# Optimization experiments

Hardware: AMD Instinct MI355X
Metric: run time of the kernel (lower is better)

Reference implementation:

```python
import jax, jax.numpy as jnp
import numpy as np

N_VARS = 1_000_000
NB, NS, NL = 400_000, 300_000, 200_000  # binary / small-int / large-int counts
C_CLS = 16
N_CON = 500_000
E = 16_000_000
LP_SOL_COL = 8
BIAS_COL = 1
LAMBDA_MEAN, LAMBDA_MAX = 1.0, 0.1


def setup_inputs() -> dict:
    key = jax.random.key(0)
    ks = jax.random.split(key, 10)
    # disjoint variable index partitions: [0,NB) bin, [NB,NB+NS) small int,
    # [NB+NS,NB+NS+NL) large int, rest continuous (var_types==0)
    idx_bin = jnp.arange(NB, dtype=jnp.int64)
    idx_int_small = jnp.arange(NB, NB + NS, dtype=jnp.int64)
    idx_int_large = jnp.arange(NB + NS, NB + NS + NL, dtype=jnp.int64)
    var_types = jnp.concatenate([
        jnp.ones(NB, dtype=jnp.int64),                 # binary
        jnp.full((NS + NL,), 2, dtype=jnp.int64),      # integer
        jnp.zeros(N_VARS - NB - NS - NL, dtype=jnp.int64),  # continuous
    ])
    edge_indices = jnp.stack([
        jax.random.randint(ks[0], (E,), 0, N_CON, dtype=jnp.int64),
        jax.random.randint(ks[1], (E,), 0, N_VARS, dtype=jnp.int64),
    ])
    return {
        'prob_bin': jax.random.uniform(ks[2], (NB, 1), jnp.float32),
        'logits_int_small': jax.random.normal(ks[3], (NS, C_CLS), jnp.float32),
        'int_small_offsets': jax.random.normal(ks[4], (NS,), jnp.float32),
        'pred_int_large': jax.random.normal(ks[5], (NL, 1), jnp.float32),
        'edge_features': jax.random.normal(ks[6], (E, 1), jnp.float32),
        'constraint_features': jax.random.normal(ks[7], (N_CON, 8), jnp.float32),
        'variable_features': jax.random.normal(ks[8], (N_VARS, 16), jnp.float32),
        'idx_bin': idx_bin,
        'idx_int_small': idx_int_small,
        'idx_int_large': idx_int_large,
        'var_types': var_types,
        'edge_indices': edge_indices,
        'n_vars': N_VARS,
    }


def _build_x(prob_bin, logits_int_small, int_small_offsets, pred_int_large,
             variable_features, idx_bin, idx_int_small, idx_int_large,
             var_types, n_vars):
    x = jnp.zeros((n_vars,), dtype=prob_bin.dtype)
    x = x.at[idx_bin].set(prob_bin[:, 0])
    # expected value of small-int class distribution
    probs = jax.nn.softmax(logits_int_small, axis=-1)                  # [NS, C]
    class_values = jnp.arange(logits_int_small.shape[1], dtype=probs.dtype)
    expected = probs @ class_values + int_small_offsets                # [NS]
    x = x.at[idx_int_small].set(expected)
    x = x.at[idx_int_large].set(pred_int_large[:, 0])
    # continuous vars take detached LP solution values
    lp_vals = jax.lax.stop_gradient(variable_features[:, LP_SOL_COL])
    x = jnp.where(var_types == 0, lp_vals, x)
    return x


def reference(prob_bin, logits_int_small, int_small_offsets, pred_int_large,
              edge_features, constraint_features, variable_features,
              idx_bin, idx_int_small, idx_int_large, var_types,
              edge_indices, n_vars):
    x = _build_x(prob_bin, logits_int_small, int_small_offsets, pred_int_large,
                 variable_features, idx_bin, idx_int_small, idx_int_large,
                 var_types, n_vars)
    n_cons = constraint_features.shape[0]
    # sparse A @ x: gather variable values along edges, scale, scatter-add per constraint
    weighted = edge_features.reshape(-1) * x[edge_indices[1]]          # [E]
    Ax = jax.ops.segment_sum(weighted, edge_indices[0], num_segments=n_cons)
    violation = jax.nn.relu(Ax - constraint_features[:, BIAS_COL])     # [N_con]
    mean_viol = violation.mean()
    max_viol = violation.max()
    n_violated = jnp.sum(violation > 1e-6)
    penalty = LAMBDA_MEAN * mean_viol + LAMBDA_MAX * max_viol
    return penalty, mean_viol, max_viol, n_violated
```

## Files before the change

### kernel.cpp

```cpp
#include <hip/hip_runtime.h>


#define BSHIFT 14
#define BROWS  (1 << BSHIFT)
#define NBUCK_MAX 32
#define CHUNK 8192
#define ROUNDS (CHUNK / 1024)
#define BUF 128
#define THRESH 48
#define SPLIT 16

typedef int   iv4 __attribute__((ext_vector_type(4)));
typedef float fv4 __attribute__((ext_vector_type(4)));

__device__ inline unsigned pack_rec(int loc, float v) {
    unsigned f = __float_as_uint(v);
    unsigned b = (f + 0x7FFFu + ((f >> 16) & 1u)) >> 16;
    return ((unsigned)loc << 16) | b;
}


__global__ __launch_bounds__(256) void k_build_hist(
    const float* __restrict__ prob_bin, const int* __restrict__ idx_bin, int NB, int gBin,
    const float* __restrict__ logits, const float* __restrict__ offs,
    const int* __restrict__ idx_small, int NS, int gSml,
    const float* __restrict__ pred, const int* __restrict__ idx_large, int NL, int gLrg,
    const int* __restrict__ vt, const float* __restrict__ vf, int NV, int gCnt,
    const int* __restrict__ rows, int* __restrict__ counts,
    int nchunks, int E, int nbuck,
    float* __restrict__ x, float* __restrict__ acc)
{
    int blk = blockIdx.x, tid = threadIdx.x;
    if (blk == 0 && tid < 4) reinterpret_cast<unsigned*>(acc)[tid] = 0u;

    if (blk < gBin) {
        int i = blk * 256 + tid;
        if (i < NB) x[idx_bin[i]] = prob_bin[i];
        return;
    }
    blk -= gBin;
    if (blk < gSml) {
        int i = blk * 256 + tid;
        if (i < NS) {
            const fv4* lp = reinterpret_cast<const fv4*>(logits + (size_t)i * 16);
            fv4 v0 = lp[0], v1 = lp[1], v2 = lp[2], v3 = lp[3];
            float l[16] = {v0.x, v0.y, v0.z, v0.w, v1.x, v1.y, v1.z, v1.w,
                           v2.x, v2.y, v2.z, v2.w, v3.x, v3.y, v3.z, v3.w};
            float m = l[0];
#pragma unroll
            for (int j = 1; j < 16; ++j) m = fmaxf(m, l[j]);
            float s = 0.f, ws = 0.f;
#pragma unroll
            for (int j = 0; j < 16; ++j) {
                float e = expf(l[j] - m);
                s += e;
                ws += e * (float)j;
            }
            x[idx_small[i]] = ws / s + offs[i];
        }
        return;
    }
    blk -= gSml;
    if (blk < gLrg) {
        int i = blk * 256 + tid;
        if (i < NL) x[idx_large[i]] = pred[i];
        return;
    }
    blk -= gLrg;
    if (blk < gCnt) {
        int v = blk * 256 + tid;
        if (v < NV && vt[v] == 0) x[v] = vf[(size_t)v * 16 + 8];
        return;
    }
    blk -= gCnt;
    __shared__ int h[NBUCK_MAX];
    if (tid < NBUCK_MAX) h[tid] = 0;
    __syncthreads();
    int e4max = E >> 2;
    int base4 = blk * (CHUNK / 4);
#pragma unroll
    for (int k = 0; k < ROUNDS; ++k) {
        int i4 = base4 + k * 256 + tid;
        if (i4 < e4max) {
            iv4 r = reinterpret_cast<const iv4*>(rows)[i4];
            atomicAdd(&h[r.x >> BSHIFT], 1);
            atomicAdd(&h[r.y >> BSHIFT], 1);
            atomicAdd(&h[r.z >> BSHIFT], 1);
            atomicAdd(&h[r.w >> BSHIFT], 1);
        }
    }
    if (blk == 0 && tid < (E & 3))
        atomicAdd(&h[rows[(E & ~3) + tid] >> BSHIFT], 1);
    __syncthreads();
    if (tid < nbuck) counts[(size_t)tid * nchunks + blk] = h[tid];
}


__global__ void k_scanchunks(const int* __restrict__ counts, int* __restrict__ off,
                             int* __restrict__ total, int nchunks) {
    int b = blockIdx.x, lane = threadIdx.x;
    int carry = 0;
    for (int i0 = 0; i0 < nchunks; i0 += 64) {
        int i = i0 + lane;
        int v = (i < nchunks) ? counts[(size_t)b * nchunks + i] : 0;
        int orig = v;
#pragma unroll
        for (int o = 1; o < 64; o <<= 1) {
            int t = __shfl_up(v, o, 64);
            if (lane >= o) v += t;
        }
        if (i < nchunks) off[(size_t)b * nchunks + i] = carry + v - orig;
        carry += __shfl(v, 63, 64);
    }
    if (lane == 0) total[b] = carry;
}

__global__ void k_bases(const int* __restrict__ total, int* __restrict__ base, int nbuck) {
    if (blockIdx.x == 0 && threadIdx.x == 0) {
        int s = 0;
        for (int b = 0; b < nbuck; ++b) { base[b] = s; s += total[b]; }
        base[nbuck] = s;
    }
}


__global__ __launch_bounds__(256) void k_scatter3(const int* __restrict__ rows,
                                                  const int* __restrict__ cols,
                                                  const float* __restrict__ ef,
                                                  const float* __restrict__ x,
                                                  const int* __restrict__ off,
                                                  const int* __restrict__ base,
                                                  unsigned* __restrict__ recs,
                                                  int nchunks, int E, int nbuck) {
    __shared__ unsigned bufr[NBUCK_MAX][BUF];
    __shared__ int fill[NBUCK_MAX];
    __shared__ int done[NBUCK_MAX];
    __shared__ int cbase[NBUCK_MAX];

    int tid = threadIdx.x, chunk = blockIdx.x;
    if (tid < NBUCK_MAX) {
        fill[tid] = 0;
        done[tid] = 0;
        cbase[tid] = (tid < nbuck) ? base[tid] + off[(size_t)tid * nchunks + chunk] : 0;
    }
    __syncthreads();

    int e4max = E >> 2;
    int base4 = chunk * (CHUNK / 4);
    int wid = tid >> 6, lane = tid & 63;

    iv4 r, c; fv4 f;
    bool valid;
    {
        int i4 = base4 + tid;
        valid = i4 < e4max;
        if (valid) {
            r = __builtin_nontemporal_load(reinterpret_cast<const iv4*>(rows) + i4);
            c = __builtin_nontemporal_load(reinterpret_cast<const iv4*>(cols) + i4);
            f = __builtin_nontemporal_load(reinterpret_cast<const fv4*>(ef) + i4);
        }
    }

    for (int k = 0; k < ROUNDS; ++k) {
        iv4 rr = r, cc = c; fv4 ff = f;
        bool val = valid;
        if (k + 1 < ROUNDS) {
            int i4 = base4 + (k + 1) * 256 + tid;
            valid = i4 < e4max;
            if (valid) {
                r = __builtin_nontemporal_load(reinterpret_cast<const iv4*>(rows) + i4);
                c = __builtin_nontemporal_load(reinterpret_cast<const iv4*>(cols) + i4);
                f = __builtin_nontemporal_load(reinterpret_cast<const fv4*>(ef) + i4);
            }
        }
        if (val) {
            int   ra[4] = {rr.x, rr.y, rr.z, rr.w};
            int   ca[4] = {cc.x, cc.y, cc.z, cc.w};
            float fa[4] = {ff.x, ff.y, ff.z, ff.w};
#pragma unroll
            for (int j = 0; j < 4; ++j) {
                int b = ra[j] >> BSHIFT;
                unsigned rec = pack_rec(ra[j] & (BROWS - 1), fa[j] * x[ca[j]]);
                int pos = atomicAdd(&fill[b], 1);
                if (pos < BUF) bufr[b][pos] = rec;
                else recs[cbase[b] + done[b] + pos] = rec;
            }
        }
        if (k == ROUNDS - 1 && chunk == 0 && tid < (E & 3)) {
            int e = (E & ~3) + tid;
            int rrow = rows[e];
            int b = rrow >> BSHIFT;
            unsigned rec = pack_rec(rrow & (BROWS - 1), ef[e] * x[cols[e]]);
            int pos = atomicAdd(&fill[b], 1);
            if (pos < BUF) bufr[b][pos] = rec;
            else recs[cbase[b] + done[b] + pos] = rec;
        }
        __syncthreads();
        bool last = (k == ROUNDS - 1);
        for (int b = wid; b < nbuck; b += 4) {
            int fl = fill[b];
            if (fl == 0) continue;
            if (fl >= THRESH || last) {
                int n = fl < BUF ? fl : BUF;
                int g = cbase[b] + done[b];
                for (int j = lane; j < n; j += 64) recs[g + j] = bufr[b][j];
                if (lane == 0) { done[b] += fl; fill[b] = 0; }
            }
        }
        __syncthreads();
    }
}


__global__ __launch_bounds__(256) void k_accum(const unsigned* __restrict__ recs,
                                               const int* __restrict__ base,
                                               float* __restrict__ partial) {
    __shared__ float tile[BROWS];
    int tid = threadIdx.x;
    int b = blockIdx.x / SPLIT, s = blockIdx.x % SPLIT;
    for (int i = tid; i < BROWS; i += 256) tile[i] = 0.f;
    __syncthreads();
    int lo = base[b], hi = base[b + 1];
    int len = hi - lo, per = (len + SPLIT - 1) / SPLIT;
    int s0 = lo + s * per;
    int s1 = s0 + per; if (s1 > hi) s1 = hi;
    int i = s0 + tid;
    for (; i + 768 < s1; i += 1024) {
        unsigned r0 = __builtin_nontemporal_load(recs + i);
        unsigned r1 = __builtin_nontemporal_load(recs + i + 256);
        unsigned r2 = __builtin_nontemporal_load(recs + i + 512);
        unsigned r3 = __builtin_nontemporal_load(recs + i + 768);
        atomicAdd(&tile[r0 >> 16], __uint_as_float((r0 & 0xFFFFu) << 16));
        atomicAdd(&tile[r1 >> 16], __uint_as_float((r1 & 0xFFFFu) << 16));
        atomicAdd(&tile[r2 >> 16], __uint_as_float((r2 & 0xFFFFu) << 16));
        atomicAdd(&tile[r3 >> 16], __uint_as_float((r3 & 0xFFFFu) << 16));
    }
    for (; i < s1; i += 256) {
        unsigned rr = recs[i];
        atomicAdd(&tile[rr >> 16], __uint_as_float((rr & 0xFFFFu) << 16));
    }
    __syncthreads();
    float* out = partial + ((size_t)blockIdx.x << BSHIFT);
    for (int j = tid; j < BROWS; j += 256) out[j] = tile[j];
}


__global__ __launch_bounds__(256) void k_reduce_fin(const float* __restrict__ partial,
                                                    const float* __restrict__ cf,
                                                    float* __restrict__ acc,
                                                    float* __restrict__ out,
                                                    int ncon, int nblocks) {
    float lsum = 0.f, lmax = 0.f;
    unsigned lcnt = 0;
    int stride = gridDim.x * blockDim.x;
    for (int c = blockIdx.x * blockDim.x + threadIdx.x; c < ncon; c += stride) {
        int b = c >> BSHIFT, i = c & (BROWS - 1);
        const float* p = partial + (((size_t)b * SPLIT) << BSHIFT) + i;
        float v = 0.f;
#pragma unroll
        for (int s = 0; s < SPLIT; ++s)
            v += __builtin_nontemporal_load(p + ((size_t)s << BSHIFT));
        v -= cf[(size_t)c * 8 + 1];
        v = v > 0.f ? v : 0.f;
        lsum += v;
        lmax = fmaxf(lmax, v);
        lcnt += (v > 1e-6f) ? 1u : 0u;
    }
#pragma unroll
    for (int o = 32; o > 0; o >>= 1) {
        lsum += __shfl_down(lsum, o);
        lmax = fmaxf(lmax, __shfl_down(lmax, o));
        lcnt += __shfl_down(lcnt, o);
    }
    __shared__ float ssum[4];
    __shared__ float smax[4];
    __shared__ unsigned scnt[4];
    int lane = threadIdx.x & 63, wid = threadIdx.x >> 6;
    if (lane == 0) { ssum[wid] = lsum; smax[wid] = lmax; scnt[wid] = lcnt; }
    __syncthreads();
    if (threadIdx.x == 0) {
        float bs = 0.f, bm = 0.f;
        unsigned bc = 0;
        int nw = (blockDim.x + 63) >> 6;
        for (int w = 0; w < nw; ++w) { bs += ssum[w]; bm = fmaxf(bm, smax[w]); bc += scnt[w]; }
        atomicAdd(&acc[0], bs);
        atomicMax(reinterpret_cast<unsigned*>(acc) + 1, __float_as_uint(bm));
        atomicAdd(reinterpret_cast<unsigned*>(acc) + 2, bc);
        __threadfence();
        unsigned t = atomicAdd(reinterpret_cast<unsigned*>(acc) + 3, 1u);
        if (t == (unsigned)(nblocks - 1)) {
            float sum   = atomicAdd(&acc[0], 0.f);
            unsigned mb = atomicMax(reinterpret_cast<unsigned*>(acc) + 1, 0u);
            unsigned ct = atomicAdd(reinterpret_cast<unsigned*>(acc) + 2, 0u);
            float mean = sum / (float)ncon;
            float mx = __uint_as_float(mb);
            out[0] = mean + 0.1f * mx;
            out[1] = mean;
            out[2] = mx;
            out[3] = (float)ct;
        }
    }
}


__global__ void k_scatter_f(const float* __restrict__ src, const int* __restrict__ idx,
                            float* __restrict__ x, int n) {
    int i = blockIdx.x * blockDim.x + threadIdx.x;
    if (i < n) x[idx[i]] = src[i];
}

__global__ void k_edges(const float* __restrict__ ef, const int* __restrict__ rows,
                        const int* __restrict__ cols, const float* __restrict__ x,
                        float* __restrict__ Ax, int e4, int E) {
    int stride = gridDim.x * blockDim.x;
    int gid = blockIdx.x * blockDim.x + threadIdx.x;
    for (int i = gid; i < e4; i += stride) {
        fv4 f = reinterpret_cast<const fv4*>(ef)[i];
        iv4 r = reinterpret_cast<const iv4*>(rows)[i];
        iv4 c = reinterpret_cast<const iv4*>(cols)[i];
        atomicAdd(&Ax[r.x], f.x * x[c.x]);
        atomicAdd(&Ax[r.y], f.y * x[c.y]);
        atomicAdd(&Ax[r.z], f.z * x[c.z]);
        atomicAdd(&Ax[r.w], f.w * x[c.w]);
    }
    for (int e = e4 * 4 + gid; e < E; e += stride)
        atomicAdd(&Ax[rows[e]], ef[e] * x[cols[e]]);
}

__global__ void k_reduce_ax(const float* __restrict__ Ax, const float* __restrict__ cf,
                            float* __restrict__ acc, int ncon) {
    float lsum = 0.f, lmax = 0.f;
    unsigned lcnt = 0;
    int stride = gridDim.x * blockDim.x;
    for (int c = blockIdx.x * blockDim.x + threadIdx.x; c < ncon; c += stride) {
        float v = Ax[c] - cf[(size_t)c * 8 + 1];
        v = v > 0.f ? v : 0.f;
        lsum += v;
        lmax = fmaxf(lmax, v);
        lcnt += (v > 1e-6f) ? 1u : 0u;
    }
#pragma unroll
    for (int o = 32; o > 0; o >>= 1) {
        lsum += __shfl_down(lsum, o);
        lmax = fmaxf(lmax, __shfl_down(lmax, o));
        lcnt += __shfl_down(lcnt, o);
    }
    __shared__ float ssum[4];
    __shared__ float smax[4];
    __shared__ unsigned scnt[4];
    int lane = threadIdx.x & 63, wid = threadIdx.x >> 6;
    if (lane == 0) { ssum[wid] = lsum; smax[wid] = lmax; scnt[wid] = lcnt; }
    __syncthreads();
    if (threadIdx.x == 0) {
        float bs = 0.f, bm = 0.f;
        unsigned bc = 0;
        int nw = (blockDim.x + 63) >> 6;
        for (int w = 0; w < nw; ++w) { bs += ssum[w]; bm = fmaxf(bm, smax[w]); bc += scnt[w]; }
        atomicAdd(&acc[0], bs);
        atomicMax(reinterpret_cast<unsigned*>(acc) + 1, __float_as_uint(bm));
        atomicAdd(reinterpret_cast<unsigned*>(acc) + 2, bc);
    }
}

__global__ void k_final(const float* __restrict__ acc, float* __restrict__ out, int ncon) {
    if (blockIdx.x == 0 && threadIdx.x == 0) {
        float sum = acc[0];
        float mx = __uint_as_float(reinterpret_cast<const unsigned*>(acc)[1]);
        unsigned cnt = reinterpret_cast<const unsigned*>(acc)[2];
        float mean = sum / (float)ncon;
        out[0] = mean + 0.1f * mx;
        out[1] = mean;
        out[2] = mx;
        out[3] = (float)cnt;
    }
}

__global__ void k_small_int_f(const float* __restrict__ logits, const float* __restrict__ offs,
                              const int* __restrict__ idx, float* __restrict__ x, int n) {
    int i = blockIdx.x * blockDim.x + threadIdx.x;
    if (i >= n) return;
    const fv4* lp = reinterpret_cast<const fv4*>(logits + (size_t)i * 16);
    fv4 v0 = lp[0], v1 = lp[1], v2 = lp[2], v3 = lp[3];
    float l[16] = {v0.x, v0.y, v0.z, v0.w, v1.x, v1.y, v1.z, v1.w,
                   v2.x, v2.y, v2.z, v2.w, v3.x, v3.y, v3.z, v3.w};
    float m = l[0];
#pragma unroll
    for (int j = 1; j < 16; ++j) m = fmaxf(m, l[j]);
    float s = 0.f, ws = 0.f;
#pragma unroll
    for (int j = 0; j < 16; ++j) {
        float e = expf(l[j] - m);
        s += e;
        ws += e * (float)j;
    }
    x[idx[i]] = ws / s + offs[i];
}

__global__ void k_continuous_f(const int* __restrict__ vt, const float* __restrict__ vf,
                               float* __restrict__ x, int n) {
    int v = blockIdx.x * blockDim.x + threadIdx.x;
    if (v < n && vt[v] == 0) x[v] = vf[(size_t)v * 16 + 8];
}


extern "C" void kernel_launch(void* const* d_in, const int* in_sizes, int n_in,
                              void* d_out, int out_size, void* d_ws, size_t ws_size,
                              hipStream_t stream) {
    const float* prob_bin     = (const float*)d_in[0];
    const float* logits_small = (const float*)d_in[1];
    const float* offs_small   = (const float*)d_in[2];
    const float* pred_large   = (const float*)d_in[3];
    const float* edge_feat    = (const float*)d_in[4];
    const float* cons_feat    = (const float*)d_in[5];
    const float* var_feat     = (const float*)d_in[6];
    const int*   idx_bin      = (const int*)d_in[7];
    const int*   idx_small    = (const int*)d_in[8];
    const int*   idx_large    = (const int*)d_in[9];
    const int*   var_types    = (const int*)d_in[10];
    const int*   edge_indices = (const int*)d_in[11];

    const int NB    = in_sizes[0];
    const int NS    = in_sizes[2];
    const int NL    = in_sizes[3];
    const int E     = in_sizes[4];
    const int NCON  = in_sizes[5] / 8;
    const int NVARS = in_sizes[10];

    const int* rows = edge_indices;
    const int* cols = edge_indices + E;

    const int nbuck   = (NCON + BROWS - 1) >> BSHIFT;
    const int nchunks = (E + CHUNK - 1) / CHUNK;

    char* w = (char*)d_ws;
    size_t o = 0;
    auto take = [&](size_t bytes) -> char* {
        char* p = w + o;
        o = (o + bytes + 255) & ~(size_t)255;
        return p;
    };
    float*    x       = (float*)take((size_t)NVARS * 4);
    unsigned* recs    = (unsigned*)take((size_t)E * 4);
    float*    partial = (float*)take((size_t)nbuck * SPLIT * BROWS * 4);
    int*      counts  = (int*)take((size_t)nbuck * nchunks * 4);
    int*      off     = (int*)take((size_t)nbuck * nchunks * 4);
    int*      base    = (int*)take((size_t)(nbuck + 1) * 4);
    int*      total   = (int*)take((size_t)nbuck * 4);
    float*    acc     = (float*)take(16);

    bool sorted_path = (o <= ws_size) && (nbuck <= NBUCK_MAX);

    const int B = 256;

    if (sorted_path) {
        const int gBin = (NB + B - 1) / B;
        const int gSml = (NS + B - 1) / B;
        const int gLrg = (NL + B - 1) / B;
        const int gCnt = (NVARS + B - 1) / B;
        const int grid1 = gBin + gSml + gLrg + gCnt + nchunks;

        k_build_hist<<<grid1, B, 0, stream>>>(
            prob_bin, idx_bin, NB, gBin,
            logits_small, offs_small, idx_small, NS, gSml,
            pred_large, idx_large, NL, gLrg,
            var_types, var_feat, NVARS, gCnt,
            rows, counts, nchunks, E, nbuck, x, acc);
        k_scanchunks<<<nbuck, 64, 0, stream>>>(counts, off, total, nchunks);
        k_bases<<<1, 64, 0, stream>>>(total, base, nbuck);
        k_scatter3<<<nchunks, B, 0, stream>>>(rows, cols, edge_feat, x, off, base,
                                              recs, nchunks, E, nbuck);
        k_accum<<<nbuck * SPLIT, B, 0, stream>>>(recs, base, partial);
        const int rblocks = 1024;
        k_reduce_fin<<<rblocks, B, 0, stream>>>(partial, cons_feat, acc, (float*)d_out,
                                                NCON, rblocks);
    } else {
        float* accf = (float*)((char*)d_ws + (size_t)NVARS * 4);
        float* Ax   = accf + 4;
        (void)hipMemsetAsync(accf, 0, (size_t)(4 + NCON) * sizeof(float), stream);
        k_scatter_f<<<(NB + B - 1) / B, B, 0, stream>>>(prob_bin, idx_bin, x, NB);
        k_small_int_f<<<(NS + B - 1) / B, B, 0, stream>>>(logits_small, offs_small, idx_small, x, NS);
        k_scatter_f<<<(NL + B - 1) / B, B, 0, stream>>>(pred_large, idx_large, x, NL);
        k_continuous_f<<<(NVARS + B - 1) / B, B, 0, stream>>>(var_types, var_feat, x, NVARS);
        k_edges<<<2048, B, 0, stream>>>(edge_feat, rows, cols, x, Ax, E / 4, E);
        k_reduce_ax<<<1024, B, 0, stream>>>(Ax, cons_feat, accf, NCON);
        k_final<<<1, 64, 0, stream>>>(accf, (float*)d_out, NCON);
    }
}
```

Measured before the change: 313.3 us.

## Compute bf16 edge products in histogram pass and scan with wide blocks

The x-building work is split out of the histogram kernel. The histogram pass now also gathers x, multiplies by the edge weights and writes packed bf16 products, so the scatter pass reads 8 bytes per 4 edges instead of re-reading cols and edge features and gathering x. The chunk scan uses 1024-thread blocks and folds in the bucket-base computation, and bucket segments are padded to multiples of 4 so the accumulate kernel can use vector loads. This adds a product buffer write and read and a second edge pass that loads cols, features and x, in exchange for a lighter scatter pass and fewer launches.

```diff
diff --git a/kernel.cpp b/kernel.cpp
--- a/kernel.cpp
+++ b/kernel.cpp
@@ -10,24 +10,23 @@
 #define THRESH 48
 #define SPLIT 16
 
-typedef int   iv4 __attribute__((ext_vector_type(4)));
-typedef float fv4 __attribute__((ext_vector_type(4)));
-
-__device__ inline unsigned pack_rec(int loc, float v) {
+typedef int      iv4 __attribute__((ext_vector_type(4)));
+typedef float    fv4 __attribute__((ext_vector_type(4)));
+typedef unsigned uv2 __attribute__((ext_vector_type(2)));
+typedef unsigned uv4 __attribute__((ext_vector_type(4)));
+
+__device__ inline unsigned bf16bits(float v) {
     unsigned f = __float_as_uint(v);
-    unsigned b = (f + 0x7FFFu + ((f >> 16) & 1u)) >> 16;
-    return ((unsigned)loc << 16) | b;
-}
-
-
-__global__ __launch_bounds__(256) void k_build_hist(
+    return (f + 0x7FFFu + ((f >> 16) & 1u)) >> 16;
+}
+
+
+__global__ __launch_bounds__(256) void k_build_x(
     const float* __restrict__ prob_bin, const int* __restrict__ idx_bin, int NB, int gBin,
     const float* __restrict__ logits, const float* __restrict__ offs,
     const int* __restrict__ idx_small, int NS, int gSml,
     const float* __restrict__ pred, const int* __restrict__ idx_large, int NL, int gLrg,
-    const int* __restrict__ vt, const float* __restrict__ vf, int NV, int gCnt,
-    const int* __restrict__ rows, int* __restrict__ counts,
-    int nchunks, int E, int nbuck,
+    const int* __restrict__ vt, const float* __restrict__ vf, int NV,
     float* __restrict__ x, float* __restrict__ acc)
 {
     int blk = blockIdx.x, tid = threadIdx.x;
@@ -67,69 +66,106 @@
         return;
     }
     blk -= gLrg;
-    if (blk < gCnt) {
+    {
         int v = blk * 256 + tid;
         if (v < NV && vt[v] == 0) x[v] = vf[(size_t)v * 16 + 8];
-        return;
-    }
-    blk -= gCnt;
-    __shared__ int h[NBUCK_MAX];
-    if (tid < NBUCK_MAX) h[tid] = 0;
+    }
+}
+
+
+template <bool PROD>
+__global__ __launch_bounds__(256) void k_hist_prod(const int* __restrict__ rows,
+                                                   const int* __restrict__ cols,
+                                                   const float* __restrict__ ef,
+                                                   const float* __restrict__ x,
+                                                   int* __restrict__ counts,
+                                                   unsigned* __restrict__ prods,
+                                                   int nchunks, int E, int nbuck) {
+    __shared__ int h[4][NBUCK_MAX];
+    int tid = threadIdx.x, chunk = blockIdx.x, wid = tid >> 6, lane = tid & 63;
+    if (lane < NBUCK_MAX) h[wid][lane] = 0;
     __syncthreads();
     int e4max = E >> 2;
-    int base4 = blk * (CHUNK / 4);
+    int b4 = chunk * (CHUNK / 4);
 #pragma unroll
     for (int k = 0; k < ROUNDS; ++k) {
-        int i4 = base4 + k * 256 + tid;
+        int i4 = b4 + k * 256 + tid;
         if (i4 < e4max) {
-            iv4 r = reinterpret_cast<const iv4*>(rows)[i4];
-            atomicAdd(&h[r.x >> BSHIFT], 1);
-            atomicAdd(&h[r.y >> BSHIFT], 1);
-            atomicAdd(&h[r.z >> BSHIFT], 1);
-            atomicAdd(&h[r.w >> BSHIFT], 1);
-        }
-    }
-    if (blk == 0 && tid < (E & 3))
-        atomicAdd(&h[rows[(E & ~3) + tid] >> BSHIFT], 1);
-    __syncthreads();
-    if (tid < nbuck) counts[(size_t)tid * nchunks + blk] = h[tid];
-}
-
-
-__global__ void k_scanchunks(const int* __restrict__ counts, int* __restrict__ off,
-                             int* __restrict__ total, int nchunks) {
-    int b = blockIdx.x, lane = threadIdx.x;
+            iv4 r = __builtin_nontemporal_load(reinterpret_cast<const iv4*>(rows) + i4);
+            atomicAdd(&h[wid][r.x >> BSHIFT], 1);
+            atomicAdd(&h[wid][r.y >> BSHIFT], 1);
+            atomicAdd(&h[wid][r.z >> BSHIFT], 1);
+            atomicAdd(&h[wid][r.w >> BSHIFT], 1);
+            if (PROD) {
+                iv4 c = __builtin_nontemporal_load(reinterpret_cast<const iv4*>(cols) + i4);
+                fv4 f = __builtin_nontemporal_load(reinterpret_cast<const fv4*>(ef) + i4);
+                unsigned p01 = bf16bits(f.x * x[c.x]) | (bf16bits(f.y * x[c.y]) << 16);
+                unsigned p23 = bf16bits(f.z * x[c.z]) | (bf16bits(f.w * x[c.w]) << 16);
+                uv2 p = {p01, p23};
+                __builtin_nontemporal_store(p, reinterpret_cast<uv2*>(prods) + i4);
+            }
+        }
+    }
+    if (chunk == 0 && tid < (E & 3)) {
+        int e = (E & ~3) + tid;
+        atomicAdd(&h[wid][rows[e] >> BSHIFT], 1);
+        if (PROD)
+            reinterpret_cast<unsigned short*>(prods)[e] =
+                (unsigned short)bf16bits(ef[e] * x[cols[e]]);
+    }
+    __syncthreads();
+    if (tid < nbuck)
+        counts[(size_t)tid * nchunks + chunk] = h[0][tid] + h[1][tid] + h[2][tid] + h[3][tid];
+}
+
+
+__global__ __launch_bounds__(1024) void k_scan(const int* __restrict__ counts,
+                                               int* __restrict__ off,
+                                               int* __restrict__ total, int nchunks) {
+    int b = blockIdx.x;
+    __shared__ int wtot[16];
+    __shared__ int wbase[16];
+    int tid = threadIdx.x, w = tid >> 6, lane = tid & 63;
+    int seg = (nchunks + 15) >> 4;
+    int lo = w * seg;
+    int hi = lo + seg; if (hi > nchunks) hi = nchunks;
+    const int* cb = counts + (size_t)b * nchunks;
+    int* ob = off + (size_t)b * nchunks;
     int carry = 0;
-    for (int i0 = 0; i0 < nchunks; i0 += 64) {
+    for (int i0 = lo; i0 < hi; i0 += 64) {
         int i = i0 + lane;
-        int v = (i < nchunks) ? counts[(size_t)b * nchunks + i] : 0;
+        int v = (i < hi) ? cb[i] : 0;
         int orig = v;
 #pragma unroll
         for (int o = 1; o < 64; o <<= 1) {
             int t = __shfl_up(v, o, 64);
             if (lane >= o) v += t;
         }
-        if (i < nchunks) off[(size_t)b * nchunks + i] = carry + v - orig;
+        if (i < hi) ob[i] = carry + v - orig;
         carry += __shfl(v, 63, 64);
     }
-    if (lane == 0) total[b] = carry;
-}
-
-__global__ void k_bases(const int* __restrict__ total, int* __restrict__ base, int nbuck) {
-    if (blockIdx.x == 0 && threadIdx.x == 0) {
+    if (lane == 0) wtot[w] = carry;
+    __syncthreads();
+    if (tid == 0) {
         int s = 0;
-        for (int b = 0; b < nbuck; ++b) { base[b] = s; s += total[b]; }
-        base[nbuck] = s;
-    }
-}
-
-
-__global__ __launch_bounds__(256) void k_scatter3(const int* __restrict__ rows,
+        for (int k = 0; k < 16; ++k) { wbase[k] = s; s += wtot[k]; }
+        total[b] = s;
+    }
+    __syncthreads();
+    int add = wbase[w];
+    if (add)
+        for (int i = lo + lane; i < hi; i += 64) ob[i] += add;
+}
+
+
+template <bool PROD>
+__global__ __launch_bounds__(256) void k_scatter5(const int* __restrict__ rows,
                                                   const int* __restrict__ cols,
                                                   const float* __restrict__ ef,
                                                   const float* __restrict__ x,
+                                                  const unsigned* __restrict__ prods,
                                                   const int* __restrict__ off,
-                                                  const int* __restrict__ base,
+                                                  const int* __restrict__ total,
                                                   unsigned* __restrict__ recs,
                                                   int nchunks, int E, int nbuck) {
     __shared__ unsigned bufr[NBUCK_MAX][BUF];
@@ -137,50 +173,59 @@
     __shared__ int done[NBUCK_MAX];
     __shared__ int cbase[NBUCK_MAX];
 
-    int tid = threadIdx.x, chunk = blockIdx.x;
-    if (tid < NBUCK_MAX) {
+    int tid = threadIdx.x, chunk = blockIdx.x, wid = tid >> 6, lane = tid & 63;
+    if (tid < 32) {
+        int t = (tid < nbuck) ? total[tid] : 0;
+        int p = (t + 3) & ~3;
+        int sc = p;
+#pragma unroll
+        for (int o = 1; o < 32; o <<= 1) {
+            int u = __shfl_up(sc, o, 64);
+            if (tid >= o) sc += u;
+        }
+        cbase[tid] = (sc - p) + ((tid < nbuck) ? off[(size_t)tid * nchunks + chunk] : 0);
         fill[tid] = 0;
         done[tid] = 0;
-        cbase[tid] = (tid < nbuck) ? base[tid] + off[(size_t)tid * nchunks + chunk] : 0;
     }
     __syncthreads();
 
     int e4max = E >> 2;
-    int base4 = chunk * (CHUNK / 4);
-    int wid = tid >> 6, lane = tid & 63;
-
-    iv4 r, c; fv4 f;
-    bool valid;
-    {
-        int i4 = base4 + tid;
-        valid = i4 < e4max;
-        if (valid) {
-            r = __builtin_nontemporal_load(reinterpret_cast<const iv4*>(rows) + i4);
-            c = __builtin_nontemporal_load(reinterpret_cast<const iv4*>(cols) + i4);
-            f = __builtin_nontemporal_load(reinterpret_cast<const fv4*>(ef) + i4);
-        }
-    }
-
+    int b4 = chunk * (CHUNK / 4);
+
+    iv4 r, c; fv4 f; uv2 p; bool v;
+#define LOADK(k)                                                              \
+    {   int i4 = b4 + (k) * 256 + tid;                                        \
+        v = i4 < e4max;                                                       \
+        if (v) {                                                              \
+            r = __builtin_nontemporal_load(reinterpret_cast<const iv4*>(rows) + i4); \
+            if (PROD) {                                                       \
+                p = __builtin_nontemporal_load(reinterpret_cast<const uv2*>(prods) + i4); \
+            } else {                                                          \
+                c = __builtin_nontemporal_load(reinterpret_cast<const iv4*>(cols) + i4); \
+                f = __builtin_nontemporal_load(reinterpret_cast<const fv4*>(ef) + i4);   \
+            }                                                                 \
+        } }
+
+    LOADK(0)
     for (int k = 0; k < ROUNDS; ++k) {
-        iv4 rr = r, cc = c; fv4 ff = f;
-        bool val = valid;
-        if (k + 1 < ROUNDS) {
-            int i4 = base4 + (k + 1) * 256 + tid;
-            valid = i4 < e4max;
-            if (valid) {
-                r = __builtin_nontemporal_load(reinterpret_cast<const iv4*>(rows) + i4);
-                c = __builtin_nontemporal_load(reinterpret_cast<const iv4*>(cols) + i4);
-                f = __builtin_nontemporal_load(reinterpret_cast<const fv4*>(ef) + i4);
+        iv4 rr = r; iv4 cc = c; fv4 ff = f; uv2 pp = p; bool vv = v;
+        if (k + 1 < ROUNDS) LOADK(k + 1)
+        if (vv) {
+            unsigned q[4];
+            if (PROD) {
+                q[0] = pp.x & 0xFFFFu; q[1] = pp.x >> 16;
+                q[2] = pp.y & 0xFFFFu; q[3] = pp.y >> 16;
+            } else {
+                q[0] = bf16bits(ff.x * x[cc.x]);
+                q[1] = bf16bits(ff.y * x[cc.y]);
+                q[2] = bf16bits(ff.z * x[cc.z]);
+                q[3] = bf16bits(ff.w * x[cc.w]);
             }
-        }
-        if (val) {
-            int   ra[4] = {rr.x, rr.y, rr.z, rr.w};
-            int   ca[4] = {cc.x, cc.y, cc.z, cc.w};
-            float fa[4] = {ff.x, ff.y, ff.z, ff.w};
+            int ra[4] = {rr.x, rr.y, rr.z, rr.w};
 #pragma unroll
             for (int j = 0; j < 4; ++j) {
                 int b = ra[j] >> BSHIFT;
-                unsigned rec = pack_rec(ra[j] & (BROWS - 1), fa[j] * x[ca[j]]);
+                unsigned rec = ((unsigned)(ra[j] & (BROWS - 1)) << 16) | q[j];
                 int pos = atomicAdd(&fill[b], 1);
                 if (pos < BUF) bufr[b][pos] = rec;
                 else recs[cbase[b] + done[b] + pos] = rec;
@@ -189,8 +234,10 @@
         if (k == ROUNDS - 1 && chunk == 0 && tid < (E & 3)) {
             int e = (E & ~3) + tid;
             int rrow = rows[e];
+            unsigned q16 = PROD ? (unsigned)reinterpret_cast<const unsigned short*>(prods)[e]
+                                : bf16bits(ef[e] * x[cols[e]]);
             int b = rrow >> BSHIFT;
-            unsigned rec = pack_rec(rrow & (BROWS - 1), ef[e] * x[cols[e]]);
+            unsigned rec = ((unsigned)(rrow & (BROWS - 1)) << 16) | q16;
             int pos = atomicAdd(&fill[b], 1);
             if (pos < BUF) bufr[b][pos] = rec;
             else recs[cbase[b] + done[b] + pos] = rec;
@@ -209,39 +256,53 @@
         }
         __syncthreads();
     }
+#undef LOADK
 }
 
 
 __global__ __launch_bounds__(256) void k_accum(const unsigned* __restrict__ recs,
-                                               const int* __restrict__ base,
-                                               float* __restrict__ partial) {
+                                               const int* __restrict__ total,
+                                               float* __restrict__ partial, int nbuck) {
     __shared__ float tile[BROWS];
+    __shared__ int sb[2];
     int tid = threadIdx.x;
     int b = blockIdx.x / SPLIT, s = blockIdx.x % SPLIT;
-    for (int i = tid; i < BROWS; i += 256) tile[i] = 0.f;
-    __syncthreads();
-    int lo = base[b], hi = base[b + 1];
-    int len = hi - lo, per = (len + SPLIT - 1) / SPLIT;
+    if (tid < 32) {
+        int t = (tid < nbuck) ? total[tid] : 0;
+        int pq = (t + 3) & ~3;
+        int sc = pq;
+#pragma unroll
+        for (int o = 1; o < 32; o <<= 1) {
+            int u = __shfl_up(sc, o, 64);
+            if (tid >= o) sc += u;
+        }
+        if (tid == b) { sb[0] = sc - pq; sb[1] = t; }
+    }
+    fv4 z = {0.f, 0.f, 0.f, 0.f};
+    for (int i = tid; i < BROWS / 4; i += 256) reinterpret_cast<fv4*>(tile)[i] = z;
+    __syncthreads();
+    int lo = sb[0], len = sb[1], hi = lo + len;
+    int per = ((len + SPLIT - 1) / SPLIT + 3) & ~3;
     int s0 = lo + s * per;
     int s1 = s0 + per; if (s1 > hi) s1 = hi;
-    int i = s0 + tid;
-    for (; i + 768 < s1; i += 1024) {
-        unsigned r0 = __builtin_nontemporal_load(recs + i);
-        unsigned r1 = __builtin_nontemporal_load(recs + i + 256);
-        unsigned r2 = __builtin_nontemporal_load(recs + i + 512);
-        unsigned r3 = __builtin_nontemporal_load(recs + i + 768);
-        atomicAdd(&tile[r0 >> 16], __uint_as_float((r0 & 0xFFFFu) << 16));
-        atomicAdd(&tile[r1 >> 16], __uint_as_float((r1 & 0xFFFFu) << 16));
-        atomicAdd(&tile[r2 >> 16], __uint_as_float((r2 & 0xFFFFu) << 16));
-        atomicAdd(&tile[r3 >> 16], __uint_as_float((r3 & 0xFFFFu) << 16));
-    }
-    for (; i < s1; i += 256) {
-        unsigned rr = recs[i];
-        atomicAdd(&tile[rr >> 16], __uint_as_float((rr & 0xFFFFu) << 16));
-    }
+    int i = s0 + (tid << 2);
+    for (; i + 3 < s1; i += 1024) {
+        uv4 r = __builtin_nontemporal_load(reinterpret_cast<const uv4*>(recs + i));
+        atomicAdd(&tile[r.x >> 16], __uint_as_float((r.x & 0xFFFFu) << 16));
+        atomicAdd(&tile[r.y >> 16], __uint_as_float((r.y & 0xFFFFu) << 16));
+        atomicAdd(&tile[r.z >> 16], __uint_as_float((r.z & 0xFFFFu) << 16));
+        atomicAdd(&tile[r.w >> 16], __uint_as_float((r.w & 0xFFFFu) << 16));
+    }
+    if (i < s1)
+        for (int j = i; j < s1; ++j) {
+            unsigned rr = recs[j];
+            atomicAdd(&tile[rr >> 16], __uint_as_float((rr & 0xFFFFu) << 16));
+        }
     __syncthreads();
     float* out = partial + ((size_t)blockIdx.x << BSHIFT);
-    for (int j = tid; j < BROWS; j += 256) out[j] = tile[j];
+    for (int j = tid; j < BROWS / 4; j += 256)
+        __builtin_nontemporal_store(reinterpret_cast<const fv4*>(tile)[j],
+                                    reinterpret_cast<fv4*>(out) + j);
 }
 
 
@@ -281,8 +342,7 @@
     if (threadIdx.x == 0) {
         float bs = 0.f, bm = 0.f;
         unsigned bc = 0;
-        int nw = (blockDim.x + 63) >> 6;
-        for (int w = 0; w < nw; ++w) { bs += ssum[w]; bm = fmaxf(bm, smax[w]); bc += scnt[w]; }
+        for (int w = 0; w < 4; ++w) { bs += ssum[w]; bm = fmaxf(bm, smax[w]); bc += scnt[w]; }
         atomicAdd(&acc[0], bs);
         atomicMax(reinterpret_cast<unsigned*>(acc) + 1, __float_as_uint(bm));
         atomicAdd(reinterpret_cast<unsigned*>(acc) + 2, bc);
@@ -303,12 +363,6 @@
 }
 
 
-__global__ void k_scatter_f(const float* __restrict__ src, const int* __restrict__ idx,
-                            float* __restrict__ x, int n) {
-    int i = blockIdx.x * blockDim.x + threadIdx.x;
-    if (i < n) x[idx[i]] = src[i];
-}
-
 __global__ void k_edges(const float* __restrict__ ef, const int* __restrict__ rows,
                         const int* __restrict__ cols, const float* __restrict__ x,
                         float* __restrict__ Ax, int e4, int E) {
@@ -328,7 +382,8 @@
 }
 
 __global__ void k_reduce_ax(const float* __restrict__ Ax, const float* __restrict__ cf,
-                            float* __restrict__ acc, int ncon) {
+                            float* __restrict__ acc, float* __restrict__ out,
+                            int ncon, int nblocks) {
     float lsum = 0.f, lmax = 0.f;
     unsigned lcnt = 0;
     int stride = gridDim.x * blockDim.x;
@@ -354,52 +409,24 @@
     if (threadIdx.x == 0) {
         float bs = 0.f, bm = 0.f;
         unsigned bc = 0;
-        int nw = (blockDim.x + 63) >> 6;
-        for (int w = 0; w < nw; ++w) { bs += ssum[w]; bm = fmaxf(bm, smax[w]); bc += scnt[w]; }
+        for (int w = 0; w < 4; ++w) { bs += ssum[w]; bm = fmaxf(bm, smax[w]); bc += scnt[w]; }
         atomicAdd(&acc[0], bs);
         atomicMax(reinterpret_cast<unsigned*>(acc) + 1, __float_as_uint(bm));
         atomicAdd(reinterpret_cast<unsigned*>(acc) + 2, bc);
-    }
-}
-
-__global__ void k_final(const float* __restrict__ acc, float* __restrict__ out, int ncon) {
-    if (blockIdx.x == 0 && threadIdx.x == 0) {
-        float sum = acc[0];
-        float mx = __uint_as_float(reinterpret_cast<const unsigned*>(acc)[1]);
-        unsigned cnt = reinterpret_cast<const unsigned*>(acc)[2];
-        float mean = sum / (float)ncon;
-        out[0] = mean + 0.1f * mx;
-        out[1] = mean;
-        out[2] = mx;
-        out[3] = (float)cnt;
-    }
-}
-
-__global__ void k_small_int_f(const float* __restrict__ logits, const float* __restrict__ offs,
-                              const int* __restrict__ idx, float* __restrict__ x, int n) {
-    int i = blockIdx.x * blockDim.x + threadIdx.x;
-    if (i >= n) return;
-    const fv4* lp = reinterpret_cast<const fv4*>(logits + (size_t)i * 16);
-    fv4 v0 = lp[0], v1 = lp[1], v2 = lp[2], v3 = lp[3];
-    float l[16] = {v0.x, v0.y, v0.z, v0.w, v1.x, v1.y, v1.z, v1.w,
-                   v2.x, v2.y, v2.z, v2.w, v3.x, v3.y, v3.z, v3.w};
-    float m = l[0];
-#pragma unroll
-    for (int j = 1; j < 16; ++j) m = fmaxf(m, l[j]);
-    float s = 0.f, ws = 0.f;
-#pragma unroll
-    for (int j = 0; j < 16; ++j) {
-        float e = expf(l[j] - m);
-        s += e;
-        ws += e * (float)j;
-    }
-    x[idx[i]] = ws / s + offs[i];
-}
-
-__global__ void k_continuous_f(const int* __restrict__ vt, const float* __restrict__ vf,
-                               float* __restrict__ x, int n) {
-    int v = blockIdx.x * blockDim.x + threadIdx.x;
-    if (v < n && vt[v] == 0) x[v] = vf[(size_t)v * 16 + 8];
+        __threadfence();
+        unsigned t = atomicAdd(reinterpret_cast<unsigned*>(acc) + 3, 1u);
+        if (t == (unsigned)(nblocks - 1)) {
+            float sum   = atomicAdd(&acc[0], 0.f);
+            unsigned mb = atomicMax(reinterpret_cast<unsigned*>(acc) + 1, 0u);
+            unsigned ct = atomicAdd(reinterpret_cast<unsigned*>(acc) + 2, 0u);
+            float mean = sum / (float)ncon;
+            float mx = __uint_as_float(mb);
+            out[0] = mean + 0.1f * mx;
+            out[1] = mean;
+            out[2] = mx;
+            out[3] = (float)ct;
+        }
+    }
 }
 
 
@@ -440,49 +467,66 @@
         return p;
     };
     float*    x       = (float*)take((size_t)NVARS * 4);
-    unsigned* recs    = (unsigned*)take((size_t)E * 4);
+    unsigned* recs    = (unsigned*)take((size_t)(E + 4 * NBUCK_MAX) * 4);
     float*    partial = (float*)take((size_t)nbuck * SPLIT * BROWS * 4);
     int*      counts  = (int*)take((size_t)nbuck * nchunks * 4);
     int*      off     = (int*)take((size_t)nbuck * nchunks * 4);
-    int*      base    = (int*)take((size_t)(nbuck + 1) * 4);
     int*      total   = (int*)take((size_t)nbuck * 4);
-    float*    acc     = (float*)take(16);
-
-    bool sorted_path = (o <= ws_size) && (nbuck <= NBUCK_MAX);
+    float*    acc     = (float*)take(32);
+    size_t needB = o;
+    unsigned* prods   = (unsigned*)take((size_t)(E / 2 + 8) * 4);
+    size_t needA = o;
 
     const int B = 256;
-
-    if (sorted_path) {
+    bool tierA = (ws_size >= needA) && (nbuck <= NBUCK_MAX);
+    bool tierB = (ws_size >= needB) && (nbuck <= NBUCK_MAX);
+
+    if (tierA || tierB) {
         const int gBin = (NB + B - 1) / B;
         const int gSml = (NS + B - 1) / B;
         const int gLrg = (NL + B - 1) / B;
         const int gCnt = (NVARS + B - 1) / B;
-        const int grid1 = gBin + gSml + gLrg + gCnt + nchunks;
-
-        k_build_hist<<<grid1, B, 0, stream>>>(
+
+        k_build_x<<<gBin + gSml + gLrg + gCnt, B, 0, stream>>>(
             prob_bin, idx_bin, NB, gBin,
             logits_small, offs_small, idx_small, NS, gSml,
             pred_large, idx_large, NL, gLrg,
-            var_types, var_feat, NVARS, gCnt,
-            rows, counts, nchunks, E, nbuck, x, acc);
-        k_scanchunks<<<nbuck, 64, 0, stream>>>(counts, off, total, nchunks);
-        k_bases<<<1, 64, 0, stream>>>(total, base, nbuck);
-        k_scatter3<<<nchunks, B, 0, stream>>>(rows, cols, edge_feat, x, off, base,
-                                              recs, nchunks, E, nbuck);
-        k_accum<<<nbuck * SPLIT, B, 0, stream>>>(recs, base, partial);
+            var_types, var_feat, NVARS, x, acc);
+
+        if (tierA)
+            k_hist_prod<true><<<nchunks, B, 0, stream>>>(rows, cols, edge_feat, x,
+                                                         counts, prods, nchunks, E, nbuck);
+        else
+            k_hist_prod<false><<<nchunks, B, 0, stream>>>(rows, cols, edge_feat, x,
+                                                          counts, prods, nchunks, E, nbuck);
+
+        k_scan<<<nbuck, 1024, 0, stream>>>(counts, off, total, nchunks);
+
+        if (tierA)
+            k_scatter5<true><<<nchunks, B, 0, stream>>>(rows, cols, edge_feat, x, prods,
+                                                        off, total, recs, nchunks, E, nbuck);
+        else
+            k_scatter5<false><<<nchunks, B, 0, stream>>>(rows, cols, edge_feat, x, prods,
+                                                         off, total, recs, nchunks, E, nbuck);
+
+        k_accum<<<nbuck * SPLIT, B, 0, stream>>>(recs, total, partial, nbuck);
         const int rblocks = 1024;
         k_reduce_fin<<<rblocks, B, 0, stream>>>(partial, cons_feat, acc, (float*)d_out,
                                                 NCON, rblocks);
     } else {
         float* accf = (float*)((char*)d_ws + (size_t)NVARS * 4);
-        float* Ax   = accf + 4;
-        (void)hipMemsetAsync(accf, 0, (size_t)(4 + NCON) * sizeof(float), stream);
-        k_scatter_f<<<(NB + B - 1) / B, B, 0, stream>>>(prob_bin, idx_bin, x, NB);
-        k_small_int_f<<<(NS + B - 1) / B, B, 0, stream>>>(logits_small, offs_small, idx_small, x, NS);
-        k_scatter_f<<<(NL + B - 1) / B, B, 0, stream>>>(pred_large, idx_large, x, NL);
-        k_continuous_f<<<(NVARS + B - 1) / B, B, 0, stream>>>(var_types, var_feat, x, NVARS);
+        float* Ax   = accf + 8;
+        (void)hipMemsetAsync(accf, 0, (size_t)(8 + NCON) * sizeof(float), stream);
+        const int gBin = (NB + B - 1) / B;
+        const int gSml = (NS + B - 1) / B;
+        const int gLrg = (NL + B - 1) / B;
+        const int gCnt = (NVARS + B - 1) / B;
+        k_build_x<<<gBin + gSml + gLrg + gCnt, B, 0, stream>>>(
+            prob_bin, idx_bin, NB, gBin,
+            logits_small, offs_small, idx_small, NS, gSml,
+            pred_large, idx_large, NL, gLrg,
+            var_types, var_feat, NVARS, x, accf);
         k_edges<<<2048, B, 0, stream>>>(edge_feat, rows, cols, x, Ax, E / 4, E);
-        k_reduce_ax<<<1024, B, 0, stream>>>(Ax, cons_feat, accf, NCON);
-        k_final<<<1, 64, 0, stream>>>(accf, (float*)d_out, NCON);
-    }
-}
+        k_reduce_ax<<<1024, B, 0, stream>>>(Ax, cons_feat, accf, (float*)d_out, NCON, 1024);
+    }
+}
```

Measured after the change: 314.7 us. About the same (+0.4%).
